# Optimization experiments

Hardware: AMD Instinct MI355X
Metric: run time of the kernel (lower is better)

## Reference

```python
import jax, jax.numpy as jnp
import numpy as np

B, L, D = 8, 4096, 256
G, K = 64, 8          # n_groups, group_size
N = G * K             # 512 slots
H = 8                 # attention heads
EPS = 1e-5

def _ln(x, g, b):
    m = jnp.mean(x, axis=-1, keepdims=True)
    v = jnp.var(x, axis=-1, keepdims=True)
    return (x - m) * jax.lax.rsqrt(v + EPS) * g + b

def _gelu(x):
    return jax.nn.gelu(x, approximate=False)  # torch nn.GELU default = exact erf

def setup_inputs() -> dict:
    key = jax.random.key(0)
    ks = jax.random.split(key, 24)
    s = 0.02
    d = {
        'X': jax.random.normal(ks[0], (B, L, D), jnp.float32),
        'S': jax.random.normal(ks[1], (B, N, D), jnp.float32),
        'Wg':  jax.random.normal(ks[2], (D, G)) * s,
        'Wk':  jax.random.normal(ks[3], (D, K)) * s,
        'Wm1': jax.random.normal(ks[4], (D, 2*D)) * s, 'bm1': jnp.zeros((2*D,)),
        'Wm2': jax.random.normal(ks[5], (2*D, D)) * s, 'bm2': jnp.zeros((D,)),
        'Wgt1': jax.random.normal(ks[6], (D, D)) * s, 'bgt1': jnp.zeros((D,)),
        'Wgt2': jax.random.normal(ks[7], (D, 1)) * s, 'bgt2': jnp.zeros((1,)),
        'Wqkv': jax.random.normal(ks[8], (D, 3*D)) * s, 'bqkv': jnp.zeros((3*D,)),
        'Wo':  jax.random.normal(ks[9], (D, D)) * s, 'bo': jnp.zeros((D,)),
        'aln_g': jnp.ones((D,)), 'aln_b': jnp.zeros((D,)),
        'Wu1': jax.random.normal(ks[10], (2*D, 2*D)) * s, 'bu1': jnp.zeros((2*D,)),
        'Wu2': jax.random.normal(ks[11], (2*D, D)) * s, 'bu2': jnp.zeros((D,)),
        'ln_g': jnp.ones((D,)), 'ln_b': jnp.zeros((D,)),
    }
    return d

def reference(X, S, Wg, Wk, Wm1, bm1, Wm2, bm2, Wgt1, bgt1, Wgt2, bgt2,
              Wqkv, bqkv, Wo, bo, aln_g, aln_b, Wu1, bu1, Wu2, bu2, ln_g, ln_b):
    # --- hierarchical routing (eval path: argmax one-hot) ---
    msg = _gelu(X @ Wm1 + bm1) @ Wm2 + bm2                 # (B,L,D)
    gate = jax.nn.sigmoid(_gelu(X @ Wgt1 + bgt1) @ Wgt2 + bgt2)  # (B,L,1)
    gm = msg * gate
    gidx = jnp.argmax(X @ Wg, axis=-1)                     # (B,L)
    kidx = jnp.argmax(X @ Wk, axis=-1)                     # (B,L)
    idx = gidx * K + kidx                                  # flat slot id in [0,N)
    full = jax.nn.one_hot(idx, N, dtype=X.dtype)           # (B,L,N)
    incoming = jnp.einsum('bln,bld->bnd', full, gm)        # (B,N,D)
    # --- slot self-attention ---
    qkv = S @ Wqkv + bqkv
    q, k, v = jnp.split(qkv, 3, axis=-1)
    dh = D // H
    q = q.reshape(B, N, H, dh); k = k.reshape(B, N, H, dh); v = v.reshape(B, N, H, dh)
    scores = jnp.einsum('bqhd,bkhd->bhqk', q, k) / jnp.sqrt(jnp.asarray(dh, X.dtype))
    attn = jax.nn.softmax(scores, axis=-1)
    o = jnp.einsum('bhqk,bkhd->bqhd', attn, v).reshape(B, N, D) @ Wo + bo
    S1 = _ln(S + o, aln_g, aln_b)
    # --- update ---
    cat = jnp.concatenate([S1, incoming], axis=-1)         # (B,N,2D)
    S2 = S1 + _gelu(cat @ Wu1 + bu1) @ Wu2 + bu2
    return _ln(S2, ln_g, ln_b)
```

## Files before the change

kernel.cpp:

```cpp
#include <hip/hip_runtime.h>

typedef __bf16 bf16_t;
typedef __bf16 bf16x8 __attribute__((ext_vector_type(8)));
typedef __bf16 bf16x4v __attribute__((ext_vector_type(4)));
typedef __bf16 bf16x2v __attribute__((ext_vector_type(2)));
typedef float f32x4 __attribute__((ext_vector_type(4)));

#define LN_EPS 1e-5f

__device__ __forceinline__ float gelu_f(float x) {
  const float xs = x * 0.70710678118654752f;
  const float ax = fabsf(xs);
  const float t = __builtin_amdgcn_rcpf(fmaf(0.3275911f, ax, 1.0f));
  float y = fmaf(t, 1.061405429f, -1.453152027f);
  y = fmaf(t, y, 1.421413741f);
  y = fmaf(t, y, -0.284496736f);
  y = fmaf(t, y, 0.254829592f);
  y *= t;
  const float e = __expf(-ax * ax);
  const float er = fmaf(-y, e, 1.0f);
  return 0.5f * x * (1.0f + copysignf(er, xs));
}

__device__ __forceinline__ void async16(const bf16_t* g, bf16_t* l) {
  __builtin_amdgcn_global_load_lds(
      (const __attribute__((address_space(1))) void*)g,
      (__attribute__((address_space(3))) void*)l, 16, 0, 0);
}

__global__ __launch_bounds__(256)
void prep_kernel(const float* __restrict__ X, const float* __restrict__ S,
                 const float* __restrict__ Wg, const float* __restrict__ Wk,
                 const float* __restrict__ Wm1, const float* __restrict__ Wgt1,
                 const float* __restrict__ Wm2, const float* __restrict__ Wqkv,
                 const float* __restrict__ Wo, const float* __restrict__ Wu1,
                 const float* __restrict__ Wu2,
                 bf16_t* __restrict__ Xb, bf16_t* __restrict__ Sb,
                 bf16_t* __restrict__ W1t, bf16_t* __restrict__ W2t,
                 bf16_t* __restrict__ Wqkvt, bf16_t* __restrict__ Wot,
                 bf16_t* __restrict__ Wu1t, bf16_t* __restrict__ Wu2t)
{
  const int bid = blockIdx.x;
  const int t = threadIdx.x;
  if (bid < 8192) {
    const int i = bid * 256 + t;
    const float4 v = ((const float4*)X)[i];
    bf16x4v o; o[0]=(bf16_t)v.x; o[1]=(bf16_t)v.y; o[2]=(bf16_t)v.z; o[3]=(bf16_t)v.w;
    ((bf16x4v*)Xb)[i] = o;
  } else if (bid < 9216) {
    const int i = (bid - 8192) * 256 + t;
    const float4 v = ((const float4*)S)[i];
    bf16x4v o; o[0]=(bf16_t)v.x; o[1]=(bf16_t)v.y; o[2]=(bf16_t)v.z; o[3]=(bf16_t)v.w;
    ((bf16x4v*)Sb)[i] = o;
  } else if (bid < 10112) {
    const int n = bid - 9216;
    const int k = t;
    float v;
    if (n < 512)      v = Wm1[k * 512 + n];
    else if (n < 768) v = Wgt1[k * 256 + (n - 512)];
    else if (n < 832) v = Wg[k * 64 + (n - 768)];
    else if (n < 840) v = Wk[k * 8 + (n - 832)];
    else              v = 0.f;
    W1t[n * 256 + k] = (bf16_t)v;
  } else if (bid < 10368) {
    const int n = bid - 10112;
    for (int k = t; k < 512; k += 256) W2t[n * 512 + k] = (bf16_t)Wm2[k * 256 + n];
  } else if (bid < 11136) {
    const int n = bid - 10368;
    Wqkvt[n * 256 + t] = (bf16_t)Wqkv[t * 768 + n];
  } else if (bid < 11392) {
    const int n = bid - 11136;
    Wot[n * 256 + t] = (bf16_t)Wo[t * 256 + n];
  } else if (bid < 11904) {
    const int n = bid - 11392;
    for (int k = t; k < 512; k += 256) Wu1t[n * 512 + k] = (bf16_t)Wu1[k * 512 + n];
  } else {
    const int n = bid - 11904;
    for (int k = t; k < 512; k += 256) Wu2t[n * 512 + k] = (bf16_t)Wu2[k * 256 + n];
  }
}

template<int MT, int EPI>
__global__ __launch_bounds__(256)
void gemm_kernel(const bf16_t* __restrict__ A, int lda,
                 const bf16_t* __restrict__ Bt, int K,
                 const float* __restrict__ bias, const float* __restrict__ bias2,
                 void* __restrict__ outp, int ldc,
                 const float* __restrict__ gate, const float* __restrict__ resid)
{
  constexpr int BM = MT * 32;
  constexpr int IA = (BM * 4) / 256;
  const int m0 = blockIdx.x * BM;
  const int n0 = blockIdx.y * 128;
  const int t = threadIdx.x;
  const int w = t >> 6;
  const int lane = t & 63;
  const int wr = w >> 1, wc = w & 1;
  const int quad = lane >> 4, l15 = lane & 15;

  __shared__ bf16_t lA[BM * 32];
  __shared__ bf16_t lB[128 * 32];

  f32x4 acc[MT][4];
#pragma unroll
  for (int mt = 0; mt < MT; ++mt)
#pragma unroll
    for (int nt = 0; nt < 4; ++nt)
      acc[mt][nt] = (f32x4){0.f, 0.f, 0.f, 0.f};

  for (int k0 = 0; k0 < K; k0 += 32) {
#pragma unroll
    for (int i = 0; i < IA; ++i) {
      const int c = i * 256 + t;
      async16(A + (size_t)(m0 + (c >> 2)) * lda + k0 + (c & 3) * 8,
              lA + (size_t)(i * 256 + (t & 192)) * 8);
    }
#pragma unroll
    for (int i = 0; i < 2; ++i) {
      const int c = i * 256 + t;
      async16(Bt + (size_t)(n0 + (c >> 2)) * K + k0 + (c & 3) * 8,
              lB + (size_t)(i * 256 + (t & 192)) * 8);
    }
    __syncthreads();
    bf16x8 af[MT], bfr[4];
    const int ko = quad * 8;
#pragma unroll
    for (int mt = 0; mt < MT; ++mt)
      af[mt] = *(const bf16x8*)&lA[(wr * MT * 16 + mt * 16 + l15) * 32 + ko];
#pragma unroll
    for (int nt = 0; nt < 4; ++nt)
      bfr[nt] = *(const bf16x8*)&lB[(wc * 64 + nt * 16 + l15) * 32 + ko];
#pragma unroll
    for (int mt = 0; mt < MT; ++mt)
#pragma unroll
      for (int nt = 0; nt < 4; ++nt)
        acc[mt][nt] = __builtin_amdgcn_mfma_f32_16x16x32_bf16(bfr[nt], af[mt], acc[mt][nt], 0, 0, 0);
    __syncthreads();
  }

#pragma unroll
  for (int mt = 0; mt < MT; ++mt) {
    const int row = m0 + wr * MT * 16 + mt * 16 + l15;
    float gt = 0.f;
    if constexpr (EPI == 7) gt = gate[row];
#pragma unroll
    for (int nt = 0; nt < 4; ++nt) {
      const int colb = n0 + wc * 64 + nt * 16 + quad * 4;
      float v0 = acc[mt][nt][0], v1 = acc[mt][nt][1];
      float v2 = acc[mt][nt][2], v3 = acc[mt][nt][3];
      if constexpr (EPI == 1) {
        if (colb < 768) {
          const float* bp = (colb < 512) ? (bias + colb) : (bias2 + (colb - 512));
          const float4 bb = *(const float4*)bp;
          v0 = gelu_f(v0 + bb.x); v1 = gelu_f(v1 + bb.y);
          v2 = gelu_f(v2 + bb.z); v3 = gelu_f(v3 + bb.w);
        }
        bf16x4v o; o[0]=(bf16_t)v0; o[1]=(bf16_t)v1; o[2]=(bf16_t)v2; o[3]=(bf16_t)v3;
        *(bf16x4v*)&((bf16_t*)outp)[(size_t)row * ldc + colb] = o;
      } else if constexpr (EPI == 3) {
        const float4 bb = *(const float4*)&bias[colb];
        bf16x4v o; o[0]=(bf16_t)(v0+bb.x); o[1]=(bf16_t)(v1+bb.y);
        o[2]=(bf16_t)(v2+bb.z); o[3]=(bf16_t)(v3+bb.w);
        *(bf16x4v*)&((bf16_t*)outp)[(size_t)row * ldc + colb] = o;
      } else if constexpr (EPI == 4) {
        const float4 bb = *(const float4*)&bias[colb];
        float4 o = make_float4(v0+bb.x, v1+bb.y, v2+bb.z, v3+bb.w);
        *(float4*)&((float*)outp)[(size_t)row * ldc + colb] = o;
      } else if constexpr (EPI == 5) {
        const float4 bb = *(const float4*)&bias[colb];
        bf16x4v o; o[0]=(bf16_t)gelu_f(v0+bb.x); o[1]=(bf16_t)gelu_f(v1+bb.y);
        o[2]=(bf16_t)gelu_f(v2+bb.z); o[3]=(bf16_t)gelu_f(v3+bb.w);
        *(bf16x4v*)&((bf16_t*)outp)[(size_t)row * ldc + colb] = o;
      } else if constexpr (EPI == 6) {
        const float4 bb = *(const float4*)&bias[colb];
        const float4 rr = *(const float4*)&resid[(size_t)row * ldc + colb];
        float4 o = make_float4(v0+bb.x+rr.x, v1+bb.y+rr.y, v2+bb.z+rr.z, v3+bb.w+rr.w);
        *(float4*)&((float*)outp)[(size_t)row * ldc + colb] = o;
      } else {
        const float4 bb = *(const float4*)&bias[colb];
        float4 o = make_float4(v0 + gt*bb.x, v1 + gt*bb.y, v2 + gt*bb.z, v3 + gt*bb.w);
        *(float4*)&((float*)outp)[(size_t)row * ldc + colb] = o;
      }
    }
  }
}

__global__ __launch_bounds__(256)
void route_kernel(const bf16_t* __restrict__ h1g1, const float* __restrict__ Wgt2,
                  const float* __restrict__ bgt2, int* __restrict__ idxb,
                  float* __restrict__ gateb, int* __restrict__ counts)
{
  const int w = threadIdx.x >> 6, lane = threadIdx.x & 63;
  const int m = blockIdx.x * 4 + w;
  const bf16_t* rowp = h1g1 + (size_t)m * 896;

  bf16x4v g4 = *(const bf16x4v*)&rowp[512 + lane * 4];
  float s = 0.f;
#pragma unroll
  for (int j = 0; j < 4; ++j) s += (float)g4[j] * Wgt2[lane * 4 + j];
#pragma unroll
  for (int off = 32; off; off >>= 1) s += __shfl_xor(s, off, 64);
  const float gate = 1.0f / (1.0f + __expf(-(s + bgt2[0])));

  float vg = (float)rowp[768 + lane];
  int ig = lane;
#pragma unroll
  for (int off = 32; off; off >>= 1) {
    const float ov = __shfl_xor(vg, off, 64);
    const int oi = __shfl_xor(ig, off, 64);
    if (ov > vg || (ov == vg && oi < ig)) { vg = ov; ig = oi; }
  }
  float vk = (lane < 8) ? (float)rowp[832 + lane] : -1e30f;
  int ik = lane;
#pragma unroll
  for (int off = 32; off; off >>= 1) {
    const float ov = __shfl_xor(vk, off, 64);
    const int oi = __shfl_xor(ik, off, 64);
    if (ov > vk || (ov == vk && oi < ik)) { vk = ov; ik = oi; }
  }
  if (lane == 0) {
    const int idx = ig * 8 + ik;
    idxb[m] = idx;
    gateb[m] = gate;
    atomicAdd(&counts[(m >> 12) * 512 + idx], 1);
  }
}

__global__ __launch_bounds__(1024)
void scan_kernel(const int* __restrict__ counts, int* __restrict__ offsets)
{
  __shared__ int tmp[1024];
  const int t = threadIdx.x;
  const int4 c = ((const int4*)counts)[t];
  const int s = c.x + c.y + c.z + c.w;
  tmp[t] = s;
  __syncthreads();
  for (int off = 1; off < 1024; off <<= 1) {
    const int v = (t >= off) ? tmp[t - off] : 0;
    __syncthreads();
    tmp[t] += v;
    __syncthreads();
  }
  const int excl = tmp[t] - s;
  int4 o; o.x = excl; o.y = excl + c.x; o.z = o.y + c.y; o.w = o.z + c.z;
  ((int4*)offsets)[t] = o;
}

__global__ __launch_bounds__(256)
void fill_kernel(const int* __restrict__ idxb, const int* __restrict__ offsets,
                 int* __restrict__ cursor, int* __restrict__ perm)
{
  const int l = blockIdx.x * 256 + threadIdx.x;
  const int bs = (l >> 12) * 512 + idxb[l];
  const int pos = atomicAdd(&cursor[bs], 1);
  perm[offsets[bs] + pos] = l;
}

__global__ __launch_bounds__(256)
void gather_kernel(const bf16_t* __restrict__ h1g1, const float* __restrict__ gateb,
                   const int* __restrict__ perm, const int* __restrict__ offsets,
                   const int* __restrict__ counts, bf16_t* __restrict__ H,
                   float* __restrict__ sumg)
{
  const int bs = blockIdx.x;
  const int t = threadIdx.x;
  const int start = offsets[bs];
  const int cnt = counts[bs];
  float a0 = 0.f, a1 = 0.f, sg = 0.f;
  for (int i = 0; i < cnt; ++i) {
    const int l = perm[start + i];
    const float g = gateb[l];
    const bf16x2v hv = *(const bf16x2v*)&h1g1[(size_t)l * 896 + t * 2];
    a0 = fmaf(g, (float)hv[0], a0);
    a1 = fmaf(g, (float)hv[1], a1);
    sg += g;
  }
  bf16x2v o; o[0] = (bf16_t)a0; o[1] = (bf16_t)a1;
  *(bf16x2v*)&H[(size_t)bs * 512 + t * 2] = o;
  if (t == 0) sumg[bs] = sg;
}

__global__ __launch_bounds__(256)
void attn_kernel(const bf16_t* __restrict__ qkv, bf16_t* __restrict__ obuf)
{
  const int bid = blockIdx.x;
  const int qc = bid & 15;
  const int h = (bid >> 4) & 7;
  const int b = bid >> 7;
  const int t = threadIdx.x;
  const int w = t >> 6, lane = t & 63;
  const int quad = lane >> 4, l15 = lane & 15;

  __shared__ bf16_t sP[32 * 520];
  __shared__ bf16_t sVt[32 * 264];
  __shared__ float sL[32];

  bf16x8 qf[2];
#pragma unroll
  for (int mt = 0; mt < 2; ++mt) {
    const int row = b * 512 + qc * 32 + mt * 16 + l15;
    qf[mt] = *(const bf16x8*)&qkv[(size_t)row * 768 + h * 32 + quad * 8];
  }
  const float scale = 0.17677669529663687f;
  for (int kt = w; kt < 32; kt += 4) {
    const int key = b * 512 + kt * 16 + l15;
    const bf16x8 kf = *(const bf16x8*)&qkv[(size_t)key * 768 + 256 + h * 32 + quad * 8];
#pragma unroll
    for (int mt = 0; mt < 2; ++mt) {
      f32x4 c = (f32x4){0.f, 0.f, 0.f, 0.f};
      c = __builtin_amdgcn_mfma_f32_16x16x32_bf16(qf[mt], kf, c, 0, 0, 0);
#pragma unroll
      for (int r = 0; r < 4; ++r)
        sP[(mt * 16 + quad * 4 + r) * 520 + kt * 16 + l15] = (bf16_t)(c[r] * scale);
    }
  }
  __syncthreads();

#pragma unroll
  for (int ri = 0; ri < 8; ++ri) {
    const int row = w * 8 + ri;
    const bf16x8 sv = *(const bf16x8*)&sP[row * 520 + lane * 8];
    float sval[8];
    float mx = -1e30f;
#pragma unroll
    for (int j = 0; j < 8; ++j) { sval[j] = (float)sv[j]; mx = fmaxf(mx, sval[j]); }
#pragma unroll
    for (int off = 32; off; off >>= 1) mx = fmaxf(mx, __shfl_xor(mx, off, 64));
    float sum = 0.f;
    bf16x8 pv;
#pragma unroll
    for (int j = 0; j < 8; ++j) { const float e = __expf(sval[j] - mx); sum += e; pv[j] = (bf16_t)e; }
#pragma unroll
    for (int off = 32; off; off >>= 1) sum += __shfl_xor(sum, off, 64);
    *(bf16x8*)&sP[row * 520 + lane * 8] = pv;
    if (lane == 0) sL[row] = sum;
  }
  __syncthreads();

  const int omt = w >> 1, ont = w & 1;
  f32x4 oacc = (f32x4){0.f, 0.f, 0.f, 0.f};
  for (int half = 0; half < 2; ++half) {
    if (half) __syncthreads();
#pragma unroll
    for (int i = 0; i < 32; ++i) {
      const int el = i * 256 + t;
      const int dh = el & 31, key = el >> 5;
      sVt[dh * 264 + key] = qkv[(size_t)(b * 512 + half * 256 + key) * 768 + 512 + h * 32 + dh];
    }
    __syncthreads();
#pragma unroll
    for (int kt = 0; kt < 8; ++kt) {
      const bf16x8 af = *(const bf16x8*)&sP[(omt * 16 + l15) * 520 + half * 256 + kt * 32 + quad * 8];
      const bf16x8 vf = *(const bf16x8*)&sVt[(ont * 16 + l15) * 264 + kt * 32 + quad * 8];
      oacc = __builtin_amdgcn_mfma_f32_16x16x32_bf16(af, vf, oacc, 0, 0, 0);
    }
  }
#pragma unroll
  for (int r = 0; r < 4; ++r) {
    const int row = omt * 16 + quad * 4 + r;
    const float val = oacc[r] / sL[row];
    obuf[(size_t)(b * 512 + qc * 32 + row) * 256 + h * 32 + ont * 16 + l15] = (bf16_t)val;
  }
}

__global__ __launch_bounds__(256)
void ln1_kernel(const float* __restrict__ S, const float* __restrict__ o2,
                const float* __restrict__ incom, const float* __restrict__ g,
                const float* __restrict__ bb, float* __restrict__ S1f,
                bf16_t* __restrict__ A4)
{
  const int w = threadIdx.x >> 6, lane = threadIdx.x & 63;
  const int row = blockIdx.x * 4 + w;
  const size_t base = (size_t)row * 256 + lane * 4;
  const float4 xs = *(const float4*)&S[base];
  const float4 xo = *(const float4*)&o2[base];
  float x[4] = {xs.x + xo.x, xs.y + xo.y, xs.z + xo.z, xs.w + xo.w};
  float sum = x[0] + x[1] + x[2] + x[3];
  float sq = x[0]*x[0] + x[1]*x[1] + x[2]*x[2] + x[3]*x[3];
#pragma unroll
  for (int off = 32; off; off >>= 1) { sum += __shfl_xor(sum, off, 64); sq += __shfl_xor(sq, off, 64); }
  const float mean = sum * 0.00390625f;
  const float var = sq * 0.00390625f - mean * mean;
  const float rstd = rsqrtf(var + LN_EPS);
  const float4 gg = *(const float4*)&g[lane * 4];
  const float4 bv = *(const float4*)&bb[lane * 4];
  float y[4];
  y[0] = (x[0]-mean)*rstd*gg.x + bv.x;
  y[1] = (x[1]-mean)*rstd*gg.y + bv.y;
  y[2] = (x[2]-mean)*rstd*gg.z + bv.z;
  y[3] = (x[3]-mean)*rstd*gg.w + bv.w;
  *(float4*)&S1f[base] = make_float4(y[0], y[1], y[2], y[3]);
  bf16x4v yb; yb[0]=(bf16_t)y[0]; yb[1]=(bf16_t)y[1]; yb[2]=(bf16_t)y[2]; yb[3]=(bf16_t)y[3];
  *(bf16x4v*)&A4[(size_t)row * 512 + lane * 4] = yb;
  const float4 ic = *(const float4*)&incom[base];
  bf16x4v ib; ib[0]=(bf16_t)ic.x; ib[1]=(bf16_t)ic.y; ib[2]=(bf16_t)ic.z; ib[3]=(bf16_t)ic.w;
  *(bf16x4v*)&A4[(size_t)row * 512 + 256 + lane * 4] = ib;
}

__global__ __launch_bounds__(256)
void ln2_kernel(const float* __restrict__ S2, const float* __restrict__ g,
                const float* __restrict__ bb, float* __restrict__ out)
{
  const int w = threadIdx.x >> 6, lane = threadIdx.x & 63;
  const int row = blockIdx.x * 4 + w;
  const size_t base = (size_t)row * 256 + lane * 4;
  const float4 xv = *(const float4*)&S2[base];
  float x[4] = {xv.x, xv.y, xv.z, xv.w};
  float sum = x[0] + x[1] + x[2] + x[3];
  float sq = x[0]*x[0] + x[1]*x[1] + x[2]*x[2] + x[3]*x[3];
#pragma unroll
  for (int off = 32; off; off >>= 1) { sum += __shfl_xor(sum, off, 64); sq += __shfl_xor(sq, off, 64); }
  const float mean = sum * 0.00390625f;
  const float var = sq * 0.00390625f - mean * mean;
  const float rstd = rsqrtf(var + LN_EPS);
  const float4 gg = *(const float4*)&g[lane * 4];
  const float4 bv = *(const float4*)&bb[lane * 4];
  float4 o;
  o.x = (x[0]-mean)*rstd*gg.x + bv.x;
  o.y = (x[1]-mean)*rstd*gg.y + bv.y;
  o.z = (x[2]-mean)*rstd*gg.z + bv.z;
  o.w = (x[3]-mean)*rstd*gg.w + bv.w;
  *(float4*)&out[base] = o;
}

extern "C" void kernel_launch(void* const* d_in, const int* in_sizes, int n_in,
                              void* d_out, int out_size, void* d_ws, size_t ws_size,
                              hipStream_t stream)
{
  (void)in_sizes; (void)n_in; (void)out_size; (void)ws_size;
  const float* X    = (const float*)d_in[0];
  const float* S    = (const float*)d_in[1];
  const float* Wg   = (const float*)d_in[2];
  const float* Wk   = (const float*)d_in[3];
  const float* Wm1  = (const float*)d_in[4];
  const float* bm1  = (const float*)d_in[5];
  const float* Wm2  = (const float*)d_in[6];
  const float* bm2  = (const float*)d_in[7];
  const float* Wgt1 = (const float*)d_in[8];
  const float* bgt1 = (const float*)d_in[9];
  const float* Wgt2 = (const float*)d_in[10];
  const float* bgt2 = (const float*)d_in[11];
  const float* Wqkv = (const float*)d_in[12];
  const float* bqkv = (const float*)d_in[13];
  const float* Wo   = (const float*)d_in[14];
  const float* bo   = (const float*)d_in[15];
  const float* alng = (const float*)d_in[16];
  const float* alnb = (const float*)d_in[17];
  const float* Wu1  = (const float*)d_in[18];
  const float* bu1  = (const float*)d_in[19];
  const float* Wu2  = (const float*)d_in[20];
  const float* bu2  = (const float*)d_in[21];
  const float* lng  = (const float*)d_in[22];
  const float* lnb  = (const float*)d_in[23];

  char* p = (char*)d_ws;
  auto carve = [&](size_t bytes) { char* r = p; p += bytes; return r; };
  bf16_t* Xb    = (bf16_t*)carve(16777216);
  bf16_t* Sb    = (bf16_t*)carve(2097152);
  bf16_t* W1t   = (bf16_t*)carve(458752);
  bf16_t* W2t   = (bf16_t*)carve(262144);
  bf16_t* Wqkvt = (bf16_t*)carve(393216);
  bf16_t* Wot   = (bf16_t*)carve(131072);
  bf16_t* Wu1t  = (bf16_t*)carve(524288);
  bf16_t* Wu2t  = (bf16_t*)carve(262144);
  bf16_t* h1g1  = (bf16_t*)carve(58720256);
  int*    idxb  = (int*)carve(131072);
  float*  gateb = (float*)carve(131072);
  float*  incom = (float*)carve(4194304);
  bf16_t* qkvb  = (bf16_t*)carve(6291456);
  bf16_t* obuf  = (bf16_t*)carve(2097152);
  float*  o2    = (float*)carve(4194304);
  float*  S1f   = (float*)carve(4194304);
  bf16_t* A4    = (bf16_t*)carve(4194304);
  bf16_t* U     = (bf16_t*)carve(4194304);
  float*  S2    = (float*)carve(4194304);
  int*    counts  = (int*)carve(16384);
  int*    offsets = (int*)carve(16384);
  int*    cursor  = (int*)carve(16384);
  int*    perm    = (int*)carve(131072);
  float*  sumg    = (float*)carve(16384);
  bf16_t* H = U;

  prep_kernel<<<12160, 256, 0, stream>>>(X, S, Wg, Wk, Wm1, Wgt1, Wm2, Wqkv, Wo, Wu1, Wu2,
                                         Xb, Sb, W1t, W2t, Wqkvt, Wot, Wu1t, Wu2t);
  hipMemsetAsync(counts, 0, 16384, stream);
  hipMemsetAsync(cursor, 0, 16384, stream);
  gemm_kernel<4,1><<<dim3(256,7), 256, 0, stream>>>(Xb, 256, W1t, 256, bm1, bgt1, h1g1, 896,
                                                    nullptr, nullptr);
  route_kernel<<<8192, 256, 0, stream>>>(h1g1, Wgt2, bgt2, idxb, gateb, counts);
  scan_kernel<<<1, 1024, 0, stream>>>(counts, offsets);
  fill_kernel<<<128, 256, 0, stream>>>(idxb, offsets, cursor, perm);
  gather_kernel<<<4096, 256, 0, stream>>>(h1g1, gateb, perm, offsets, counts, H, sumg);
  gemm_kernel<2,7><<<dim3(64,2), 256, 0, stream>>>(H, 512, W2t, 512, bm2, nullptr, incom, 256,
                                                   sumg, nullptr);
  gemm_kernel<2,3><<<dim3(64,6), 256, 0, stream>>>(Sb, 256, Wqkvt, 256, bqkv, nullptr, qkvb, 768,
                                                   nullptr, nullptr);
  attn_kernel<<<1024, 256, 0, stream>>>(qkvb, obuf);
  gemm_kernel<2,4><<<dim3(64,2), 256, 0, stream>>>(obuf, 256, Wot, 256, bo, nullptr, o2, 256,
                                                   nullptr, nullptr);
  ln1_kernel<<<1024, 256, 0, stream>>>(S, o2, incom, alng, alnb, S1f, A4);
  gemm_kernel<2,5><<<dim3(64,4), 256, 0, stream>>>(A4, 512, Wu1t, 512, bu1, nullptr, U, 512,
                                                   nullptr, nullptr);
  gemm_kernel<2,6><<<dim3(64,2), 256, 0, stream>>>(U, 512, Wu2t, 512, bu2, nullptr, S2, 256,
                                                   nullptr, S1f);
  ln2_kernel<<<1024, 256, 0, stream>>>(S2, lng, lnb, (float*)d_out);
}
```

Baseline: 294.1 us.

## Widen GEMM K-tile with XOR-swizzled LDS, faster erf GELU, smaller M tiles

```diff
diff --git a/kernel.cpp b/kernel.cpp
--- a/kernel.cpp
+++ b/kernel.cpp
@@ -8,18 +8,36 @@
 
 #define LN_EPS 1e-5f
 
+__device__ __forceinline__ float erf_fast(float a) {
+  const float t = fabsf(a);
+  const float s = a * a;
+  float r;
+  if (t > 0.921875f) {
+    float u;
+    r = fmaf(-1.72853470e-5f, t, 3.83197126e-4f);
+    u = fmaf(-3.88396438e-3f, t, 2.42546219e-2f);
+    r = fmaf(r, s, u);
+    r = fmaf(r, t, 1.06777877e-1f);
+    r = fmaf(r, t, -6.37245935e-1f);
+    r = fmaf(r, t, -1.28717512e-1f);
+    r = fmaf(r, t, t);
+    r = 1.0f - __expf(-r * 1.442695041f * 0.693147181f);
+    r = copysignf(r, a);
+  } else {
+    r = -5.96761703e-4f;
+    r = fmaf(r, s, 4.99119423e-3f);
+    r = fmaf(r, s, -2.67681349e-2f);
+    r = fmaf(r, s, 1.12819925e-1f);
+    r = fmaf(r, s, -3.76125336e-1f);
+    r = fmaf(r, s, 1.28379166e-1f);
+    r = fmaf(r, a, a);
+  }
+  return r;
+}
+
 __device__ __forceinline__ float gelu_f(float x) {
-  const float xs = x * 0.70710678118654752f;
-  const float ax = fabsf(xs);
-  const float t = __builtin_amdgcn_rcpf(fmaf(0.3275911f, ax, 1.0f));
-  float y = fmaf(t, 1.061405429f, -1.453152027f);
-  y = fmaf(t, y, 1.421413741f);
-  y = fmaf(t, y, -0.284496736f);
-  y = fmaf(t, y, 0.254829592f);
-  y *= t;
-  const float e = __expf(-ax * ax);
-  const float er = fmaf(-y, e, 1.0f);
-  return 0.5f * x * (1.0f + copysignf(er, xs));
+  const float h = 0.5f * x;
+  return fmaf(h, erf_fast(x * 0.70710678118654752f), h);
 }
 
 __device__ __forceinline__ void async16(const bf16_t* g, bf16_t* l) {
@@ -89,7 +107,9 @@
                  const float* __restrict__ gate, const float* __restrict__ resid)
 {
   constexpr int BM = MT * 32;
-  constexpr int IA = (BM * 4) / 256;
+  constexpr int BK = 64;
+  constexpr int IA = (BM * BK) / 2048;
+  constexpr int IB = (128 * BK) / 2048;
   const int m0 = blockIdx.x * BM;
   const int n0 = blockIdx.y * 128;
   const int t = threadIdx.x;
@@ -98,8 +118,8 @@
   const int wr = w >> 1, wc = w & 1;
   const int quad = lane >> 4, l15 = lane & 15;
 
-  __shared__ bf16_t lA[BM * 32];
-  __shared__ bf16_t lB[128 * 32];
+  __shared__ bf16_t lA[BM * BK];
+  __shared__ bf16_t lB[128 * BK];
 
   f32x4 acc[MT][4];
 #pragma unroll
@@ -108,33 +128,41 @@
     for (int nt = 0; nt < 4; ++nt)
       acc[mt][nt] = (f32x4){0.f, 0.f, 0.f, 0.f};
 
-  for (int k0 = 0; k0 < K; k0 += 32) {
+  for (int k0 = 0; k0 < K; k0 += BK) {
 #pragma unroll
     for (int i = 0; i < IA; ++i) {
       const int c = i * 256 + t;
-      async16(A + (size_t)(m0 + (c >> 2)) * lda + k0 + (c & 3) * 8,
+      const int row = c >> 3, p = c & 7;
+      async16(A + (size_t)(m0 + row) * lda + k0 + ((p ^ (row & 7)) << 3),
               lA + (size_t)(i * 256 + (t & 192)) * 8);
     }
 #pragma unroll
-    for (int i = 0; i < 2; ++i) {
+    for (int i = 0; i < IB; ++i) {
       const int c = i * 256 + t;
-      async16(Bt + (size_t)(n0 + (c >> 2)) * K + k0 + (c & 3) * 8,
+      const int row = c >> 3, p = c & 7;
+      async16(Bt + (size_t)(n0 + row) * K + k0 + ((p ^ (row & 7)) << 3),
               lB + (size_t)(i * 256 + (t & 192)) * 8);
     }
     __syncthreads();
-    bf16x8 af[MT], bfr[4];
-    const int ko = quad * 8;
-#pragma unroll
-    for (int mt = 0; mt < MT; ++mt)
-      af[mt] = *(const bf16x8*)&lA[(wr * MT * 16 + mt * 16 + l15) * 32 + ko];
-#pragma unroll
-    for (int nt = 0; nt < 4; ++nt)
-      bfr[nt] = *(const bf16x8*)&lB[(wc * 64 + nt * 16 + l15) * 32 + ko];
-#pragma unroll
-    for (int mt = 0; mt < MT; ++mt)
-#pragma unroll
-      for (int nt = 0; nt < 4; ++nt)
-        acc[mt][nt] = __builtin_amdgcn_mfma_f32_16x16x32_bf16(bfr[nt], af[mt], acc[mt][nt], 0, 0, 0);
+#pragma unroll
+    for (int ksub = 0; ksub < 2; ++ksub) {
+      bf16x8 af[MT], bfr[4];
+#pragma unroll
+      for (int mt = 0; mt < MT; ++mt) {
+        const int row = wr * MT * 16 + mt * 16 + l15;
+        af[mt] = *(const bf16x8*)&lA[row * BK + ((((ksub << 2) | quad) ^ (row & 7)) << 3)];
+      }
+#pragma unroll
+      for (int nt = 0; nt < 4; ++nt) {
+        const int row = wc * 64 + nt * 16 + l15;
+        bfr[nt] = *(const bf16x8*)&lB[row * BK + ((((ksub << 2) | quad) ^ (row & 7)) << 3)];
+      }
+#pragma unroll
+      for (int mt = 0; mt < MT; ++mt)
+#pragma unroll
+        for (int nt = 0; nt < 4; ++nt)
+          acc[mt][nt] = __builtin_amdgcn_mfma_f32_16x16x32_bf16(bfr[nt], af[mt], acc[mt][nt], 0, 0, 0);
+    }
     __syncthreads();
   }
 
@@ -475,33 +503,32 @@
   bf16_t* U     = (bf16_t*)carve(4194304);
   float*  S2    = (float*)carve(4194304);
   int*    counts  = (int*)carve(16384);
+  int*    cursor  = (int*)carve(16384);
   int*    offsets = (int*)carve(16384);
-  int*    cursor  = (int*)carve(16384);
   int*    perm    = (int*)carve(131072);
   float*  sumg    = (float*)carve(16384);
   bf16_t* H = U;
 
   prep_kernel<<<12160, 256, 0, stream>>>(X, S, Wg, Wk, Wm1, Wgt1, Wm2, Wqkv, Wo, Wu1, Wu2,
                                          Xb, Sb, W1t, W2t, Wqkvt, Wot, Wu1t, Wu2t);
-  hipMemsetAsync(counts, 0, 16384, stream);
-  hipMemsetAsync(cursor, 0, 16384, stream);
+  hipMemsetAsync(counts, 0, 32768, stream);
   gemm_kernel<4,1><<<dim3(256,7), 256, 0, stream>>>(Xb, 256, W1t, 256, bm1, bgt1, h1g1, 896,
                                                     nullptr, nullptr);
   route_kernel<<<8192, 256, 0, stream>>>(h1g1, Wgt2, bgt2, idxb, gateb, counts);
   scan_kernel<<<1, 1024, 0, stream>>>(counts, offsets);
   fill_kernel<<<128, 256, 0, stream>>>(idxb, offsets, cursor, perm);
   gather_kernel<<<4096, 256, 0, stream>>>(h1g1, gateb, perm, offsets, counts, H, sumg);
-  gemm_kernel<2,7><<<dim3(64,2), 256, 0, stream>>>(H, 512, W2t, 512, bm2, nullptr, incom, 256,
-                                                   sumg, nullptr);
-  gemm_kernel<2,3><<<dim3(64,6), 256, 0, stream>>>(Sb, 256, Wqkvt, 256, bqkv, nullptr, qkvb, 768,
-                                                   nullptr, nullptr);
+  gemm_kernel<1,7><<<dim3(128,2), 256, 0, stream>>>(H, 512, W2t, 512, bm2, nullptr, incom, 256,
+                                                    sumg, nullptr);
+  gemm_kernel<1,3><<<dim3(128,6), 256, 0, stream>>>(Sb, 256, Wqkvt, 256, bqkv, nullptr, qkvb, 768,
+                                                    nullptr, nullptr);
   attn_kernel<<<1024, 256, 0, stream>>>(qkvb, obuf);
-  gemm_kernel<2,4><<<dim3(64,2), 256, 0, stream>>>(obuf, 256, Wot, 256, bo, nullptr, o2, 256,
-                                                   nullptr, nullptr);
+  gemm_kernel<1,4><<<dim3(128,2), 256, 0, stream>>>(obuf, 256, Wot, 256, bo, nullptr, o2, 256,
+                                                    nullptr, nullptr);
   ln1_kernel<<<1024, 256, 0, stream>>>(S, o2, incom, alng, alnb, S1f, A4);
-  gemm_kernel<2,5><<<dim3(64,4), 256, 0, stream>>>(A4, 512, Wu1t, 512, bu1, nullptr, U, 512,
-                                                   nullptr, nullptr);
-  gemm_kernel<2,6><<<dim3(64,2), 256, 0, stream>>>(U, 512, Wu2t, 512, bu2, nullptr, S2, 256,
-                                                   nullptr, S1f);
+  gemm_kernel<1,5><<<dim3(128,4), 256, 0, stream>>>(A4, 512, Wu1t, 512, bu1, nullptr, U, 512,
+                                                    nullptr, nullptr);
+  gemm_kernel<1,6><<<dim3(128,2), 256, 0, stream>>>(U, 512, Wu2t, 512, bu2, nullptr, S2, 256,
+                                                    nullptr, S1f);
   ln2_kernel<<<1024, 256, 0, stream>>>(S2, lng, lnb, (float*)d_out);
 }
```

After: 289.8 us. About the same (-1.5%).
